# Performance work log

Hardware: AMD Instinct MI355X
Metric: run time of the kernel (lower is better)

Reference implementation:

```python
import jax, jax.numpy as jnp
import numpy as np

B = 262144

def _init_linear(key, out_f, in_f):
    k1, k2 = jax.random.split(key)
    bound = 1.0 / np.sqrt(in_f)
    W = jax.random.uniform(k1, (out_f, in_f), jnp.float32, -bound, bound)
    b = jax.random.uniform(k2, (out_f,), jnp.float32, -bound, bound)
    return W, b

def setup_inputs() -> dict:
    key = jax.random.key(0)
    ks = jax.random.split(key, 7)
    x = jax.random.normal(ks[0], (B, 440), jnp.float32)
    bW1, bb1 = _init_linear(ks[1], 40, 40)
    bW2, bb2 = _init_linear(ks[2], 40, 40)
    bW3, bb3 = _init_linear(ks[3], 10, 40)
    sW1, sb1 = _init_linear(ks[4], 41, 41)
    sW2, sb2 = _init_linear(ks[5], 41, 41)
    sW3, sb3 = _init_linear(ks[6], 22, 41)
    return dict(x=x, bW1=bW1, bb1=bb1, bW2=bW2, bb2=bb2, bW3=bW3, bb3=bb3,
                sW1=sW1, sb1=sb1, sW2=sW2, sb2=sb2, sW3=sW3, sb3=sb3)

def reference(x, bW1, bb1, bW2, bb2, bW3, bb3, sW1, sb1, sW2, sb2, sW3, sb3):
    x_iabs = x[:, 0:40]                     # [B,40]
    x_ues = x[:, 40:].reshape(-1, 10, 40)   # [B,10,40] (one 40-dim block per segment)
    # big tower: Linear-ReLU-Linear-ReLU-Linear-Softmax
    h = jax.nn.relu(x_iabs @ bW1.T + bb1)
    h = jax.nn.relu(h @ bW2.T + bb2)
    iab = jax.nn.softmax(h @ bW3.T + bb3, axis=1)        # [B,10]
    # vectorized over the 10 segments: concat UE block with its IAB scalar
    small_in = jnp.concatenate([x_ues, iab[:, :, None]], axis=-1)  # [B,10,41]
    g = jax.nn.relu(jnp.einsum('bsi,oi->bso', small_in, sW1) + sb1)
    g = jax.nn.relu(jnp.einsum('bsi,oi->bso', g, sW2) + sb2)
    g = jax.nn.softmax(jnp.einsum('bsi,oi->bso', g, sW3) + sb3, axis=-1)  # [B,10,22]
    return g * iab[:, :, None]              # [B,10,22]
```

## Files before the change

kernel.cpp:

```cpp
#include <hip/hip_runtime.h>

typedef __attribute__((ext_vector_type(4))) float f32x4;
typedef __attribute__((ext_vector_type(8))) short s16x8;
typedef unsigned int u32;
typedef unsigned short ushort;

#define XDIM 440
#define ODIM 220
#define RPB  128
#define TPB  512
#define AW   68

__device__ __forceinline__ u32 cvtpk(float a, float b){
    u32 r; asm("v_cvt_pk_bf16_f32 %0, %1, %2" : "=v"(r) : "v"(a), "v"(b)); return r;
}
__device__ __forceinline__ void split8pk(const float* v, s16x8& h, s16x8& l){
    uint4 hu, lu; u32* hp=(u32*)&hu; u32* lp=(u32*)&lu;
    #pragma unroll
    for (int j=0;j<4;++j){
        u32 hk = cvtpk(v[2*j], v[2*j+1]);
        float h0 = __builtin_bit_cast(float, hk<<16);
        float h1 = __builtin_bit_cast(float, hk & 0xFFFF0000u);
        lp[j] = cvtpk(v[2*j]-h0, v[2*j+1]-h1);
        hp[j] = hk;
    }
    h = __builtin_bit_cast(s16x8,hu); l = __builtin_bit_cast(s16x8,lu);
}
__device__ __forceinline__ void ldsplit(const float* p, s16x8& h, s16x8& l){
    float a[8];
    *(float4*)(a)   = *(const float4*)(p);
    *(float4*)(a+4) = *(const float4*)(p+4);
    split8pk(a,h,l);
}
__device__ __forceinline__ s16x8 ld8u(const ushort* p){ return *(const s16x8*)p; }

__device__ __forceinline__ f32x4 mm3(s16x8 ah, s16x8 al, s16x8 bh, s16x8 bl, f32x4 c){
    c = __builtin_amdgcn_mfma_f32_16x16x32_bf16(ah, bh, c, 0, 0, 0);
    c = __builtin_amdgcn_mfma_f32_16x16x32_bf16(ah, bl, c, 0, 0, 0);
    c = __builtin_amdgcn_mfma_f32_16x16x32_bf16(al, bh, c, 0, 0, 0);
    return c;
}

__device__ __forceinline__ ushort bf_rne(float f){
    unsigned u = __builtin_bit_cast(unsigned, f);
    return (ushort)((u + 0x7FFFu + ((u >> 16) & 1u)) >> 16);
}

__global__ void prep_w(const float* __restrict__ bW1, const float* __restrict__ bW2,
                       const float* __restrict__ bW3, const float* __restrict__ sW1,
                       const float* __restrict__ sW2, const float* __restrict__ sW3,
                       const float* __restrict__ bb1, const float* __restrict__ bb2,
                       const float* __restrict__ bb3, const float* __restrict__ sb1,
                       const float* __restrict__ sb2, const float* __restrict__ sb3,
                       ushort* __restrict__ WH, ushort* __restrict__ WL,
                       float* __restrict__ BIAS, ushort* __restrict__ WF)
{
    int i = blockIdx.x * 256 + threadIdx.x;
    if (i < 15360) {
        int n = i >> 6, k = i & 63;
        float w = 0.f;
        if      (n < 48)  { int r = n;     if (r < 40 && k < 40) w = bW1[r*40+k]; }
        else if (n < 96)  { int r = n-48;  if (r < 40 && k < 40) w = bW2[r*40+k]; }
        else if (n < 112) { int r = n-96;  if (r < 10 && k < 40) w = bW3[r*40+k]; }
        else if (n < 160) { int r = n-112; if (r < 41 && k < 41) w = sW1[r*41+k]; }
        else if (n < 208) { int r = n-160; if (r < 41 && k < 41) w = sW2[r*41+k]; }
        else              { int r = n-208; if (r < 22 && k < 41) w = sW3[r*41+k]; }
        ushort h = bf_rne(w);
        float hf = __builtin_bit_cast(float, ((unsigned)h) << 16);
        WH[i] = h; WL[i] = bf_rne(w - hf);
    } else if (i < 15600) {
        int n = i - 15360;
        float b;
        if      (n < 48)  b = (n     < 40) ? bb1[n]     : 0.f;
        else if (n < 96)  b = (n-48  < 40) ? bb2[n-48]  : 0.f;
        else if (n < 112) b = (n-96  < 10) ? bb3[n-96]  : -1e30f;
        else if (n < 160) b = (n-112 < 41) ? sb1[n-112] : 0.f;
        else if (n < 208) b = (n-160 < 41) ? sb2[n-160] : 0.f;
        else              b = (n-208 < 22) ? sb3[n-208] : -1e30f;
        BIAS[n] = b;
    } else if (i < 31984) {
        int e = i - 15600;
        int fragid = e >> 9, rem = e & 511;
        int lane = rem >> 3, j = rem & 7;
        int t2 = fragid >> 2, ks = (fragid >> 1) & 1, half = fragid & 1;
        int li = lane & 15, q = lane >> 4;
        int r = t2*16 + li;
        int k = ks*32 + q*8 + j;
        float w = 0.f;
        if      (r < 48) { if (r < 41 && k < 41)            w = sW1[r*41+k]; }
        else if (r < 96) { int rr=r-48; if (rr<41 && k<41)  w = sW2[rr*41+k]; }
        else             { int rr=r-96; if (rr<22 && k<41)  w = sW3[rr*41+k]; }
        ushort h = bf_rne(w);
        ushort v;
        if (half == 0) v = h;
        else { float hf = __builtin_bit_cast(float, ((unsigned)h)<<16); v = bf_rne(w - hf); }
        WF[fragid*512 + lane*8 + j] = v;
    }
}

__global__ __launch_bounds__(TPB, 4) void ran5(
    const float* __restrict__ x,
    const ushort* __restrict__ WH, const ushort* __restrict__ WL,
    const float* __restrict__ BIASg, const ushort* __restrict__ WFg,
    float* __restrict__ out, int nrow)
{
    __shared__ ushort Wlds[16384];
    __shared__ float  Act[RPB][AW];
    __shared__ float  ia[RPB][10];
    __shared__ float  biasS[240];

    const int tid = threadIdx.x;
    const int l   = tid & 63;
    const int w   = tid >> 6;
    const int q   = l >> 4;
    const int li  = l & 15;
    const int w16 = w * 16;
    const int R0  = blockIdx.x * RPB;
    const int arow = w16 + li;
    const int growC = min(R0 + arow, nrow - 1);

    {
        const u32* src = (const u32*)WFg;
        u32* dst = (u32*)Wlds;
        for (int i = tid; i < 8192; i += TPB) dst[i] = src[i];
    }
    for (int i = tid; i < 240; i += TPB) biasS[i] = BIASg[i];
    for (int i = tid; i < RPB*20; i += TPB) Act[i/20][48 + i%20] = 0.f;
    __syncthreads();

#define WFRAG(t2,ks,hf) (*(const s16x8*)&Wlds[(((t2)*2+(ks))*2+(hf))*512 + l*8])

    {
        const float* xp = x + (size_t)growC * XDIM;
        float a0[8], a1[8];
        *(float4*)(a0)   = *(const float4*)(xp + q*8);
        *(float4*)(a0+4) = *(const float4*)(xp + q*8 + 4);
        if (q == 0){
            *(float4*)(a1)   = *(const float4*)(xp + 32);
            *(float4*)(a1+4) = *(const float4*)(xp + 36);
        } else {
            #pragma unroll
            for (int j=0;j<8;++j) a1[j] = 0.f;
        }
        s16x8 ah0,al0,ah1,al1;
        split8pk(a0, ah0, al0); split8pk(a1, ah1, al1);
        #pragma unroll
        for (int nt=0; nt<3; ++nt){
            int n = nt*16 + li; float b = biasS[n];
            f32x4 acc = {b,b,b,b};
            acc = mm3(ah0,al0, ld8u(WH+n*64+q*8),    ld8u(WL+n*64+q*8),    acc);
            acc = mm3(ah1,al1, ld8u(WH+n*64+32+q*8), ld8u(WL+n*64+32+q*8), acc);
            #pragma unroll
            for (int r=0;r<4;++r)
                Act[w16+q*4+r][nt*16+li] = fmaxf(acc[r],0.f);
        }
    }
    {
        s16x8 ah0,al0,ah1,al1;
        ldsplit(&Act[arow][q*8],    ah0, al0);
        ldsplit(&Act[arow][32+q*8], ah1, al1);
        #pragma unroll
        for (int nt=0; nt<3; ++nt){
            int n = 48+nt*16+li; float b = biasS[n];
            f32x4 acc = {b,b,b,b};
            acc = mm3(ah0,al0, ld8u(WH+n*64+q*8),    ld8u(WL+n*64+q*8),    acc);
            acc = mm3(ah1,al1, ld8u(WH+n*64+32+q*8), ld8u(WL+n*64+32+q*8), acc);
            #pragma unroll
            for (int r=0;r<4;++r)
                Act[w16+q*4+r][nt*16+li] = fmaxf(acc[r],0.f);
        }
    }
    {
        s16x8 ah0,al0,ah1,al1;
        ldsplit(&Act[arow][q*8],    ah0, al0);
        ldsplit(&Act[arow][32+q*8], ah1, al1);
        int n = 96+li; float b = biasS[n];
        f32x4 acc = {b,b,b,b};
        acc = mm3(ah0,al0, ld8u(WH+n*64+q*8),    ld8u(WL+n*64+q*8),    acc);
        acc = mm3(ah1,al1, ld8u(WH+n*64+32+q*8), ld8u(WL+n*64+32+q*8), acc);
        #pragma unroll
        for (int r=0;r<4;++r){
            float v = acc[r];
            float m = v;
            m = fmaxf(m, __shfl_xor(m,1)); m = fmaxf(m, __shfl_xor(m,2));
            m = fmaxf(m, __shfl_xor(m,4)); m = fmaxf(m, __shfl_xor(m,8));
            float e = __expf(v - m);
            float sum = e;
            sum += __shfl_xor(sum,1); sum += __shfl_xor(sum,2);
            sum += __shfl_xor(sum,4); sum += __shfl_xor(sum,8);
            float p = __fdividef(e, sum);
            if (li < 10) ia[w16+q*4+r][li] = p;
        }
    }

    const float* xrow = x + (size_t)growC * XDIM + 40;
    auto stage_load = [&](int S, float* pf0, float* pf1){
        const float* xp = xrow + S*40;
        *(float4*)(pf0)   = *(const float4*)(xp + q*8);
        *(float4*)(pf0+4) = *(const float4*)(xp + q*8 + 4);
        if (q == 0){
            *(float4*)(pf1)   = *(const float4*)(xp + 32);
            *(float4*)(pf1+4) = *(const float4*)(xp + 36);
        }
    };

    auto compute_slot = [&](int s, const float* pf0, const float* pf1){
        s16x8 ah0,al0,ah1,al1;
        split8pk(pf0, ah0, al0);
        float a1v[8];
        #pragma unroll
        for (int j=0;j<8;++j) a1v[j] = (q==0) ? pf1[j] : 0.f;
        if (q == 1) a1v[0] = ia[arow][s];
        split8pk(a1v, ah1, al1);
        #pragma unroll
        for (int nt=0; nt<3; ++nt){
            float b = biasS[112+nt*16+li];
            f32x4 acc = {b,b,b,b};
            acc = mm3(ah0,al0, WFRAG(nt,0,0), WFRAG(nt,0,1), acc);
            acc = mm3(ah1,al1, WFRAG(nt,1,0), WFRAG(nt,1,1), acc);
            #pragma unroll
            for (int r=0;r<4;++r)
                Act[w16+q*4+r][nt*16+li] = fmaxf(acc[r],0.f);
        }
        ldsplit(&Act[arow][q*8],    ah0, al0);
        ldsplit(&Act[arow][32+q*8], ah1, al1);
        #pragma unroll
        for (int nt=0; nt<3; ++nt){
            float b = biasS[160+nt*16+li];
            f32x4 acc = {b,b,b,b};
            acc = mm3(ah0,al0, WFRAG(3+nt,0,0), WFRAG(3+nt,0,1), acc);
            acc = mm3(ah1,al1, WFRAG(3+nt,1,0), WFRAG(3+nt,1,1), acc);
            #pragma unroll
            for (int r=0;r<4;++r)
                Act[w16+q*4+r][nt*16+li] = fmaxf(acc[r],0.f);
        }
        ldsplit(&Act[arow][q*8],    ah0, al0);
        ldsplit(&Act[arow][32+q*8], ah1, al1);
        float b6 = biasS[208+li], b7 = biasS[224+li];
        f32x4 a6 = {b6,b6,b6,b6}, a7 = {b7,b7,b7,b7};
        a6 = mm3(ah0,al0, WFRAG(6,0,0), WFRAG(6,0,1), a6);
        a6 = mm3(ah1,al1, WFRAG(6,1,0), WFRAG(6,1,1), a6);
        a7 = mm3(ah0,al0, WFRAG(7,0,0), WFRAG(7,0,1), a7);
        a7 = mm3(ah1,al1, WFRAG(7,1,0), WFRAG(7,1,1), a7);
        #pragma unroll
        for (int r=0;r<4;++r){
            float v0 = a6[r], v1 = a7[r];
            float m = fmaxf(v0, v1);
            m = fmaxf(m, __shfl_xor(m,1)); m = fmaxf(m, __shfl_xor(m,2));
            m = fmaxf(m, __shfl_xor(m,4)); m = fmaxf(m, __shfl_xor(m,8));
            float e0 = __expf(v0 - m), e1 = __expf(v1 - m);
            float sum = e0 + e1;
            sum += __shfl_xor(sum,1); sum += __shfl_xor(sum,2);
            sum += __shfl_xor(sum,4); sum += __shfl_xor(sum,8);
            int lr = w16 + q*4 + r;
            float sc = __fdividef(ia[lr][s], sum);
            Act[lr][li] = e0 * sc;
            if (li < 6) Act[lr][16 + li] = e1 * sc;
        }
        #pragma unroll
        for (int it = 0; it < 3; ++it){
            int i = l + 64*it;
            if (i < 176){
                int lr = i/11, pc = i - lr*11;
                if (R0 + w16 + lr < nrow)
                    *(float2*)(out + (size_t)(R0+w16+lr)*ODIM + s*22 + pc*2)
                        = *(const float2*)&Act[w16+lr][pc*2];
            }
        }
    };

    float pfA0[8], pfA1[8], pfB0[8], pfB1[8];
    stage_load(0, pfA0, pfA1);
    #pragma unroll 1
    for (int s = 0; s < 10; s += 2){
        stage_load(s+1, pfB0, pfB1);
        compute_slot(s, pfA0, pfA1);
        if (s+2 < 10) stage_load(s+2, pfA0, pfA1);
        compute_slot(s+1, pfB0, pfB1);
    }
#undef WFRAG
}

extern "C" void kernel_launch(void* const* d_in, const int* in_sizes, int n_in,
                              void* d_out, int out_size, void* d_ws, size_t ws_size,
                              hipStream_t stream)
{
    (void)n_in; (void)out_size; (void)ws_size;
    const float* x   = (const float*)d_in[0];
    const float* bW1 = (const float*)d_in[1];
    const float* bb1 = (const float*)d_in[2];
    const float* bW2 = (const float*)d_in[3];
    const float* bb2 = (const float*)d_in[4];
    const float* bW3 = (const float*)d_in[5];
    const float* bb3 = (const float*)d_in[6];
    const float* sW1 = (const float*)d_in[7];
    const float* sb1 = (const float*)d_in[8];
    const float* sW2 = (const float*)d_in[9];
    const float* sb2 = (const float*)d_in[10];
    const float* sW3 = (const float*)d_in[11];
    const float* sb3 = (const float*)d_in[12];
    float* outp = (float*)d_out;

    ushort* WH  = (ushort*)d_ws;
    ushort* WL  = WH + 15360;
    float*  BIAS= (float*)((char*)d_ws + 61440);
    ushort* WF  = (ushort*)((char*)d_ws + 62464);

    const int rows = in_sizes[0] / XDIM;

    prep_w<<<125, 256, 0, stream>>>(bW1, bW2, bW3, sW1, sW2, sW3,
                                    bb1, bb2, bb3, sb1, sb2, sb3,
                                    WH, WL, BIAS, WF);

    const int grid = (rows + RPB - 1) / RPB;
    ran5<<<grid, TPB, 0, stream>>>(x, WH, WL, BIAS, WF, outp, rows);
}
```

Measured before the change: 292.4 us.

## Compact small-tower weight fragments in LDS and shrink block to raise occupancy

Repacks the small-tower weight fragments so the second K-slice (k 32..40, mostly padding) is stored compactly with a padded per-lane stride instead of full 512-element fragments. This cuts the LDS weight footprint. Rows per block and threads per block drop to 112 and 448, and the activation buffer narrows. Together these are meant to fit more blocks per CU. The trade-offs are extra tail rows, a full zero-init of the activation and ia buffers, and possible LDS bank conflicts from the new 136-element stride.

```diff
diff --git a/kernel.cpp b/kernel.cpp
--- a/kernel.cpp
+++ b/kernel.cpp
@@ -7,9 +7,9 @@
 
 #define XDIM 440
 #define ODIM 220
-#define RPB  128
-#define TPB  512
-#define AW   68
+#define RPB  112
+#define TPB  448
+#define AW   52
 
 __device__ __forceinline__ u32 cvtpk(float a, float b){
     u32 r; asm("v_cvt_pk_bf16_f32 %0, %1, %2" : "=v"(r) : "v"(a), "v"(b)); return r;
@@ -78,33 +78,51 @@
         else if (n < 208) b = (n-160 < 41) ? sb2[n-160] : 0.f;
         else              b = (n-208 < 22) ? sb3[n-208] : -1e30f;
         BIAS[n] = b;
-    } else if (i < 31984) {
+    } else if (i < 23792) {
         int e = i - 15600;
         int fragid = e >> 9, rem = e & 511;
         int lane = rem >> 3, j = rem & 7;
-        int t2 = fragid >> 2, ks = (fragid >> 1) & 1, half = fragid & 1;
-        int li = lane & 15, q = lane >> 4;
+        int t2 = fragid >> 1, hf2 = fragid & 1;
+        int li = lane & 15, qq = lane >> 4;
         int r = t2*16 + li;
-        int k = ks*32 + q*8 + j;
+        int k = qq*8 + j;
         float w = 0.f;
-        if      (r < 48) { if (r < 41 && k < 41)            w = sW1[r*41+k]; }
-        else if (r < 96) { int rr=r-48; if (rr<41 && k<41)  w = sW2[rr*41+k]; }
-        else             { int rr=r-96; if (rr<22 && k<41)  w = sW3[rr*41+k]; }
+        if      (r < 48) { if (r < 41)           w = sW1[r*41+k]; }
+        else if (r < 96) { int rr=r-48; if (rr<41) w = sW2[rr*41+k]; }
+        else             { int rr=r-96; if (rr<22) w = sW3[rr*41+k]; }
         ushort h = bf_rne(w);
-        ushort v;
-        if (half == 0) v = h;
-        else { float hf = __builtin_bit_cast(float, ((unsigned)h)<<16); v = bf_rne(w - hf); }
-        WF[fragid*512 + lane*8 + j] = v;
-    }
-}
-
-__global__ __launch_bounds__(TPB, 4) void ran5(
+        ushort v = h;
+        if (hf2){ float hfv = __builtin_bit_cast(float, ((unsigned)h)<<16); v = bf_rne(w - hfv); }
+        WF[e] = v;
+    } else if (i < 28280) {
+        int e = i - 23792;
+        int lane = e / 136, c = e % 136;
+        ushort v = 0;
+        if (lane < 32 && c < 128){
+            int fragid = c >> 3, j = c & 7;
+            int t2 = fragid >> 1, hf2 = fragid & 1;
+            int li = lane & 15, qq = (lane >> 4) & 1;
+            int r = t2*16 + li;
+            int k = 32 + qq*8 + j;
+            float w = 0.f;
+            if      (r < 48) { if (r<41 && k<41)            w = sW1[r*41+k]; }
+            else if (r < 96) { int rr=r-48; if (rr<41 && k<41) w = sW2[rr*41+k]; }
+            else             { int rr=r-96; if (rr<22 && k<41) w = sW3[rr*41+k]; }
+            ushort h = bf_rne(w);
+            v = h;
+            if (hf2){ float hfv = __builtin_bit_cast(float, ((unsigned)h)<<16); v = bf_rne(w - hfv); }
+        }
+        WF[8192 + e] = v;
+    }
+}
+
+__global__ __launch_bounds__(TPB, 4) void ran6(
     const float* __restrict__ x,
     const ushort* __restrict__ WH, const ushort* __restrict__ WL,
     const float* __restrict__ BIASg, const ushort* __restrict__ WFg,
     float* __restrict__ out, int nrow)
 {
-    __shared__ ushort Wlds[16384];
+    __shared__ ushort Wlds[12680];
     __shared__ float  Act[RPB][AW];
     __shared__ float  ia[RPB][10];
     __shared__ float  biasS[240];
@@ -118,17 +136,20 @@
     const int R0  = blockIdx.x * RPB;
     const int arow = w16 + li;
     const int growC = min(R0 + arow, nrow - 1);
+    const int wb1 = 8192 + ((l < 32) ? l*136 : 4352);
 
     {
         const u32* src = (const u32*)WFg;
         u32* dst = (u32*)Wlds;
-        for (int i = tid; i < 8192; i += TPB) dst[i] = src[i];
+        for (int i = tid; i < 6340; i += TPB) dst[i] = src[i];
     }
     for (int i = tid; i < 240; i += TPB) biasS[i] = BIASg[i];
-    for (int i = tid; i < RPB*20; i += TPB) Act[i/20][48 + i%20] = 0.f;
+    for (int i = tid; i < RPB*AW; i += TPB) ((float*)Act)[i] = 0.f;
+    for (int i = tid; i < RPB*10; i += TPB) ((float*)ia)[i] = 0.f;
     __syncthreads();
 
-#define WFRAG(t2,ks,hf) (*(const s16x8*)&Wlds[(((t2)*2+(ks))*2+(hf))*512 + l*8])
+#define WF0(t2,hf) (*(const s16x8*)&Wlds[((t2)*2+(hf))*512 + l*8])
+#define WF1(t2,hf) (*(const s16x8*)&Wlds[wb1 + ((t2)*2+(hf))*8])
 
     {
         const float* xp = x + (size_t)growC * XDIM;
@@ -216,8 +237,8 @@
         for (int nt=0; nt<3; ++nt){
             float b = biasS[112+nt*16+li];
             f32x4 acc = {b,b,b,b};
-            acc = mm3(ah0,al0, WFRAG(nt,0,0), WFRAG(nt,0,1), acc);
-            acc = mm3(ah1,al1, WFRAG(nt,1,0), WFRAG(nt,1,1), acc);
+            acc = mm3(ah0,al0, WF0(nt,0), WF0(nt,1), acc);
+            acc = mm3(ah1,al1, WF1(nt,0), WF1(nt,1), acc);
             #pragma unroll
             for (int r=0;r<4;++r)
                 Act[w16+q*4+r][nt*16+li] = fmaxf(acc[r],0.f);
@@ -228,8 +249,8 @@
         for (int nt=0; nt<3; ++nt){
             float b = biasS[160+nt*16+li];
             f32x4 acc = {b,b,b,b};
-            acc = mm3(ah0,al0, WFRAG(3+nt,0,0), WFRAG(3+nt,0,1), acc);
-            acc = mm3(ah1,al1, WFRAG(3+nt,1,0), WFRAG(3+nt,1,1), acc);
+            acc = mm3(ah0,al0, WF0(3+nt,0), WF0(3+nt,1), acc);
+            acc = mm3(ah1,al1, WF1(3+nt,0), WF1(3+nt,1), acc);
             #pragma unroll
             for (int r=0;r<4;++r)
                 Act[w16+q*4+r][nt*16+li] = fmaxf(acc[r],0.f);
@@ -238,10 +259,10 @@
         ldsplit(&Act[arow][32+q*8], ah1, al1);
         float b6 = biasS[208+li], b7 = biasS[224+li];
         f32x4 a6 = {b6,b6,b6,b6}, a7 = {b7,b7,b7,b7};
-        a6 = mm3(ah0,al0, WFRAG(6,0,0), WFRAG(6,0,1), a6);
-        a6 = mm3(ah1,al1, WFRAG(6,1,0), WFRAG(6,1,1), a6);
-        a7 = mm3(ah0,al0, WFRAG(7,0,0), WFRAG(7,0,1), a7);
-        a7 = mm3(ah1,al1, WFRAG(7,1,0), WFRAG(7,1,1), a7);
+        a6 = mm3(ah0,al0, WF0(6,0), WF0(6,1), a6);
+        a6 = mm3(ah1,al1, WF1(6,0), WF1(6,1), a6);
+        a7 = mm3(ah0,al0, WF0(7,0), WF0(7,1), a7);
+        a7 = mm3(ah1,al1, WF1(7,0), WF1(7,1), a7);
         #pragma unroll
         for (int r=0;r<4;++r){
             float v0 = a6[r], v1 = a7[r];
@@ -278,7 +299,8 @@
         if (s+2 < 10) stage_load(s+2, pfA0, pfA1);
         compute_slot(s+1, pfB0, pfB1);
     }
-#undef WFRAG
+#undef WF0
+#undef WF1
 }
 
 extern "C" void kernel_launch(void* const* d_in, const int* in_sizes, int n_in,
@@ -308,10 +330,10 @@
 
     const int rows = in_sizes[0] / XDIM;
 
-    prep_w<<<125, 256, 0, stream>>>(bW1, bW2, bW3, sW1, sW2, sW3,
+    prep_w<<<111, 256, 0, stream>>>(bW1, bW2, bW3, sW1, sW2, sW3,
                                     bb1, bb2, bb3, sb1, sb2, sb3,
                                     WH, WL, BIAS, WF);
 
     const int grid = (rows + RPB - 1) / RPB;
-    ran5<<<grid, TPB, 0, stream>>>(x, WH, WL, BIAS, WF, outp, rows);
-}
+    ran6<<<grid, TPB, 0, stream>>>(x, WH, WL, BIAS, WF, outp, rows);
+}
```

New measurement: 331.6 us. +13.4%, slower.
